# Optimization experiments

Measured on AMD Instinct MI355X. Metric: run time of the kernel, lower is better.

## Reference

```python
import jax, jax.numpy as jnp
import numpy as np

N_HEAD = 16
NEG = -1.0e9


def setup_inputs() -> dict:
    key = jax.random.key(0)
    k1, k2, k3 = jax.random.split(key, 3)
    B, T, C = 4, 2048, 1024
    x = jax.random.normal(k1, (B, T, C), dtype=jnp.float32)
    # torch Linear(C, 3C, bias=False): weight [3C, C], y = x @ W.T
    w_attn = jax.random.normal(k2, (3 * C, C), dtype=jnp.float32) * (1.0 / np.sqrt(C))
    w_proj = jax.random.normal(k3, (C, C), dtype=jnp.float32) * (1.0 / np.sqrt(C))
    return {"x": x, "w_attn": w_attn, "w_proj": w_proj}


def reference(x, w_attn, w_proj):
    B, T, C = x.shape
    hd = C // N_HEAD
    qkv = x @ w_attn.T  # [B,T,3C]
    q, k, v = jnp.split(qkv, 3, axis=2)
    # [B,T,C] -> [B,H,T,hd]
    q = q.reshape(B, T, N_HEAD, hd).transpose(0, 2, 1, 3)
    k = k.reshape(B, T, N_HEAD, hd).transpose(0, 2, 1, 3)
    v = v.reshape(B, T, N_HEAD, hd).transpose(0, 2, 1, 3)
    att = jnp.einsum('bhqd,bhkd->bhqk', q, k) * (1.0 / np.sqrt(hd))
    causal = jnp.tril(jnp.ones((T, T), dtype=bool))
    att = jnp.where(causal[None, None, :, :], att, NEG)
    att = jax.nn.softmax(att, axis=-1)
    y = jnp.einsum('bhqk,bhkd->bhqd', att, v)  # [B,H,T,hd]
    y = y.transpose(0, 2, 1, 3).reshape(B, T, C)
    return y @ w_proj.T
```

## Files before the change

kernel.cpp:

```cpp
#include <hip/hip_runtime.h>
#include <hip/hip_bf16.h>

typedef __bf16 bf16x8_t __attribute__((ext_vector_type(8)));
typedef __bf16 bf16x4_t __attribute__((ext_vector_type(4)));
typedef float f32x4_t __attribute__((ext_vector_type(4)));

__device__ __forceinline__ void gload_lds16(const void* g, void* l) {
    __builtin_amdgcn_global_load_lds((const __attribute__((address_space(1))) void*)g,
                                     (__attribute__((address_space(3))) void*)l, 16, 0, 0);
}

__global__ void f2bf3_kernel(const float* __restrict__ x, const float* __restrict__ wa,
                             const float* __restrict__ wp, __bf16* __restrict__ xb,
                             __bf16* __restrict__ wab, __bf16* __restrict__ wpb) {
    int i = blockIdx.x * blockDim.x + threadIdx.x;
    const float* in; __bf16* out; int off;
    if (i < 2097152)      { in = x;  out = xb;  off = i; }
    else if (i < 2883584) { in = wa; out = wab; off = i - 2097152; }
    else                  { in = wp; out = wpb; off = i - 2883584; }
    float4 v = *(const float4*)(in + off * 4);
    bf16x4_t o;
    o[0] = (__bf16)v.x; o[1] = (__bf16)v.y; o[2] = (__bf16)v.z; o[3] = (__bf16)v.w;
    *(bf16x4_t*)(out + off * 4) = o;
}

__global__ __launch_bounds__(512, 2) void gemm1_m201(const __bf16* __restrict__ A,
                                                     const __bf16* __restrict__ Bt,
                                                     __bf16* __restrict__ Cqk,
                                                     __bf16* __restrict__ Vg,
                                                     int M, int N, int K) {
    __shared__ __bf16 As[2][256 * 64];
    __shared__ __bf16 Bs[2][256 * 64];

    const int tid  = threadIdx.x;
    const int lane = tid & 63;
    const int wid  = tid >> 6;
    const int wm   = wid >> 2;
    const int wn   = wid & 3;

    int fl = blockIdx.x;
    fl = (fl & 7) * (gridDim.x >> 3) + (fl >> 3);
    const int m0 = (fl / 12) * 256;
    const int n0 = (fl % 12) * 256;

    const int lr = lane & 15;
    const int lg = lane >> 4;
    const int cr = lg * 4;
    const int srow = lane >> 3;
    const int gcol = (((lane & 7) ^ srow) << 3);

    f32x4_t acc[8][4];
#pragma unroll
    for (int i = 0; i < 8; ++i)
#pragma unroll
        for (int j = 0; j < 4; ++j)
            acc[i][j] = (f32x4_t){0.f, 0.f, 0.f, 0.f};

    const int NT = K >> 6;
    const int NI = NT >> 1;

    bf16x8_t af[4][2], bf0[2][2], bf1[2][2];

    auto stA = [&](int kt, int buf, int half) {
        const __bf16* Ab = A + (size_t)m0 * K + (size_t)kt * 64;
        const int s0 = half * 16 + wid, s1 = s0 + 8;
        gload_lds16(Ab + (size_t)(s0 * 8 + srow) * K + gcol, &As[buf][s0 * 512]);
        gload_lds16(Ab + (size_t)(s1 * 8 + srow) * K + gcol, &As[buf][s1 * 512]);
    };
    auto stB = [&](int kt, int buf, int half) {
        const __bf16* Bb = Bt + (size_t)n0 * K + (size_t)kt * 64;
        const int s0 = half * 16 + wid, s1 = s0 + 8;
        gload_lds16(Bb + (size_t)(s0 * 8 + srow) * K + gcol, &Bs[buf][s0 * 512]);
        gload_lds16(Bb + (size_t)(s1 * 8 + srow) * K + gcol, &Bs[buf][s1 * 512]);
    };
    auto dsA = [&](const __bf16* Ab, int mfh) {
#pragma unroll
        for (int mf = 0; mf < 4; ++mf)
#pragma unroll
            for (int kk = 0; kk < 2; ++kk) {
                const int row = wm * 128 + (mfh * 4 + mf) * 16 + lr;
                const int g   = kk * 4 + lg;
                af[mf][kk] = *(const bf16x8_t*)&Ab[row * 64 + ((g ^ (row & 7)) << 3)];
            }
    };
    auto dsB = [&](const __bf16* Bb, int nfh, bf16x8_t (&dst)[2][2]) {
#pragma unroll
        for (int nfp = 0; nfp < 2; ++nfp)
#pragma unroll
            for (int kk = 0; kk < 2; ++kk) {
                const int row = wn * 64 + (nfh * 2 + nfp) * 16 + lr;
                const int g   = kk * 4 + lg;
                dst[nfp][kk] = *(const bf16x8_t*)&Bb[row * 64 + ((g ^ (row & 7)) << 3)];
            }
    };
    auto MF = [&](int mfh, bf16x8_t (&bfr)[2][2], int nfh) {
        __builtin_amdgcn_s_setprio(1);
#pragma unroll
        for (int mf = 0; mf < 4; ++mf)
#pragma unroll
            for (int nfp = 0; nfp < 2; ++nfp) {
                const int ai = mfh * 4 + mf, bi = nfh * 2 + nfp;
                acc[ai][bi] = __builtin_amdgcn_mfma_f32_16x16x32_bf16(af[mf][0], bfr[nfp][0], acc[ai][bi], 0, 0, 0);
                acc[ai][bi] = __builtin_amdgcn_mfma_f32_16x16x32_bf16(af[mf][1], bfr[nfp][1], acc[ai][bi], 0, 0, 0);
            }
        __builtin_amdgcn_s_setprio(0);
    };

#define BAR() __builtin_amdgcn_s_barrier()
#define LGK0() asm volatile("s_waitcnt lgkmcnt(0)" ::: "memory")

    stA(0, 0, 0); stA(0, 0, 1); stB(0, 0, 0); stB(0, 0, 1);
    stB(1, 1, 0); stB(1, 1, 1);
    asm volatile("s_waitcnt vmcnt(4)" ::: "memory");
    BAR();

    for (int it = 0; it < NI; ++it) {
        const int t1 = 2 * it + 1, t2 = 2 * it + 2, t3 = 2 * it + 3;
        const bool lastit = (it == NI - 1);

        dsA(As[0], 0); dsB(Bs[0], 0, bf0);
        stA(t1, 1, 0);
        BAR(); LGK0();
        MF(0, bf0, 0);
        BAR();

        dsB(Bs[0], 1, bf1);
        stA(t1, 1, 1);
        BAR(); LGK0();
        MF(0, bf1, 1);
        BAR();

        dsA(As[0], 1);
        if (!lastit) stB(t2, 0, 0);
        BAR(); LGK0();
        MF(1, bf0, 0);
        BAR();

        if (!lastit) stB(t2, 0, 1);
        if (lastit) asm volatile("s_waitcnt vmcnt(0)" ::: "memory");
        else        asm volatile("s_waitcnt vmcnt(4)" ::: "memory");
        BAR();
        MF(1, bf1, 1);
        BAR();

        dsA(As[1], 0); dsB(Bs[1], 0, bf0);
        if (!lastit) stA(t2, 0, 0);
        BAR(); LGK0();
        MF(0, bf0, 0);
        BAR();

        dsB(Bs[1], 1, bf1);
        if (!lastit) stA(t2, 0, 1);
        BAR(); LGK0();
        MF(0, bf1, 1);
        BAR();

        dsA(As[1], 1);
        if (!lastit) stB(t3, 1, 0);
        BAR(); LGK0();
        MF(1, bf0, 0);
        BAR();

        if (!lastit) stB(t3, 1, 1);
        if (lastit) asm volatile("s_waitcnt vmcnt(0)" ::: "memory");
        else        asm volatile("s_waitcnt vmcnt(4)" ::: "memory");
        BAR();
        MF(1, bf1, 1);
        BAR();
    }
#undef BAR
#undef LGK0

    if (n0 < 2048) {
#pragma unroll
        for (int mf = 0; mf < 8; ++mf)
#pragma unroll
            for (int nf = 0; nf < 4; ++nf)
#pragma unroll
                for (int r = 0; r < 4; ++r) {
                    int row = m0 + wm * 128 + mf * 16 + cr + r;
                    int col = n0 + wn * 64 + nf * 16 + lr;
                    Cqk[(size_t)row * 2048 + col] = (__bf16)acc[mf][nf][r];
                }
    } else {
#pragma unroll
        for (int mf = 0; mf < 8; ++mf) {
            const int row0 = m0 + wm * 128 + mf * 16 + cr;
            const int bb   = row0 >> 11;
            const int tt   = row0 & 2047;
#pragma unroll
            for (int nf = 0; nf < 4; ++nf) {
                const int c3 = n0 + wn * 64 + nf * 16 + lr - 2048;
                const int hh = c3 >> 6, dd = c3 & 63;
                bf16x4_t pv;
#pragma unroll
                for (int r = 0; r < 4; ++r) pv[r] = (__bf16)acc[mf][nf][r];
                *(bf16x4_t*)&Vg[((size_t)(bb * 16 + hh) * 64 + dd) * 2048 + tt] = pv;
            }
        }
    }
}

template <typename OutT>
__global__ __launch_bounds__(256) void gemm_bt(const __bf16* __restrict__ A,
                                               const __bf16* __restrict__ Bt,
                                               OutT* __restrict__ C,
                                               int M, int N, int K) {
    __shared__ __bf16 As[128 * 32];
    __shared__ __bf16 Bs[128 * 32];

    const int tid  = threadIdx.x;
    const int lane = tid & 63;
    const int wid  = tid >> 6;
    const int wm   = wid >> 1;
    const int wn   = wid & 1;

    const int nwg = gridDim.x * gridDim.y;
    int fl = blockIdx.y * gridDim.x + blockIdx.x;
    fl = (fl & 7) * (nwg >> 3) + (fl >> 3);
    const int m0 = (fl / gridDim.x) * 128;
    const int n0 = (fl % gridDim.x) * 128;

    const int lr = lane & 15;
    const int lk = (lane >> 4) * 8;
    const int cr = (lane >> 4) * 4;

    f32x4_t acc[4][4];
    for (int i = 0; i < 4; ++i)
        for (int j = 0; j < 4; ++j)
            acc[i][j] = (f32x4_t){0.f, 0.f, 0.f, 0.f};

    for (int k0 = 0; k0 < K; k0 += 32) {
        __syncthreads();
        for (int i = 0; i < 2; ++i) {
            int flat = i * 256 + tid;
            int row  = flat >> 2;
            int col  = (flat & 3) * 8;
            gload_lds16(&A[(size_t)(m0 + row) * K + k0 + col], &As[(size_t)(i * 256 + wid * 64) * 8]);
            gload_lds16(&Bt[(size_t)(n0 + row) * K + k0 + col], &Bs[(size_t)(i * 256 + wid * 64) * 8]);
        }
        __syncthreads();

        bf16x8_t af[4], bfr[4];
        for (int mf = 0; mf < 4; ++mf)
            af[mf] = *(const bf16x8_t*)&As[(wm * 64 + mf * 16 + lr) * 32 + lk];
        for (int nf = 0; nf < 4; ++nf)
            bfr[nf] = *(const bf16x8_t*)&Bs[(wn * 64 + nf * 16 + lr) * 32 + lk];
        for (int mf = 0; mf < 4; ++mf)
            for (int nf = 0; nf < 4; ++nf)
                acc[mf][nf] = __builtin_amdgcn_mfma_f32_16x16x32_bf16(af[mf], bfr[nf], acc[mf][nf], 0, 0, 0);
    }

    for (int mf = 0; mf < 4; ++mf)
        for (int nf = 0; nf < 4; ++nf)
            for (int r = 0; r < 4; ++r) {
                int row = m0 + wm * 64 + mf * 16 + cr + r;
                int col = n0 + wn * 64 + nf * 16 + lr;
                C[(size_t)row * N + col] = (OutT)acc[mf][nf][r];
            }
}

__global__ __launch_bounds__(512, 4) void attn_kernel(const __bf16* __restrict__ qkv,
                                                      const __bf16* __restrict__ Vg,
                                                      __bf16* __restrict__ y) {
    const int T = 2048, LD = 2048;
    const int orig = blockIdx.x;
    const int bidx = ((orig & 7) << 6) + (orig >> 3);
    const int pair = bidx & 7;
    const int h    = (bidx >> 3) & 15;
    const int b    = bidx >> 7;

    __shared__ __bf16 Ks[128 * 64];
    __shared__ __bf16 Vt[64 * 128];
    __shared__ __bf16 Ps[8 * 16 * 136];

    const int tid  = threadIdx.x;
    const int lane = tid & 63;
    const int w    = tid >> 6;
    const int lr   = lane & 15;
    const int lg   = lane >> 4;
    const int lk   = lg * 8;

    const __bf16* qg  = qkv + (size_t)b * T * LD + h * 64;
    const __bf16* kg  = qg + 1024;
    const __bf16* Vgb = Vg + (size_t)(b * 16 + h) * 64 * 2048;

    const float CE    = 0.125f * 1.44269504f;
    const float DEFER = 44.0f;

    const int r0    = tid >> 3;
    const int kcol  = (tid & 7) * 8;
    const int kslot = ((tid & 7) ^ (r0 & 7)) << 3;
    const int vd  = tid >> 3;
    const int vc0 = tid & 7;

    __bf16* Pw = &Ps[w * 16 * 136];

    for (int pass = 0; pass < 2; ++pass) {
        const int qs  = pass ? 15 - pair : pair;
        const int qt0 = qs * 128;
        const int nt  = qs + 1;

        bf16x8_t qf0, qf1;
        {
            const __bf16* qrow = qg + (size_t)(qt0 + w * 16 + lr) * LD;
            qf0 = *(const bf16x8_t*)&qrow[lk];
            qf1 = *(const bf16x8_t*)&qrow[32 + lk];
        }

        bf16x8_t ka = *(const bf16x8_t*)&kg[(size_t)r0 * LD + kcol];
        bf16x8_t kb = *(const bf16x8_t*)&kg[(size_t)(64 + r0) * LD + kcol];
        bf16x8_t va = *(const bf16x8_t*)&Vgb[(size_t)vd * 2048 + vc0 * 8];
        bf16x8_t vb = *(const bf16x8_t*)&Vgb[(size_t)vd * 2048 + (vc0 + 8) * 8];

        f32x4_t o_acc[4];
#pragma unroll
        for (int i = 0; i < 4; ++i) o_acc[i] = (f32x4_t){0.f, 0.f, 0.f, 0.f};
        float m_r = -3.0e38f, l_r = 0.f;

        for (int t = 0; t < nt; ++t) {
            __syncthreads();

            *(bf16x8_t*)&Ks[r0 * 64 + kslot] = ka;
            *(bf16x8_t*)&Ks[(64 + r0) * 64 + kslot] = kb;
            *(bf16x8_t*)&Vt[vd * 128 + ((vc0 ^ (vd & 7)) << 3)] = va;
            *(bf16x8_t*)&Vt[vd * 128 + (((vc0 + 8) ^ (vd & 7)) << 3)] = vb;

            __syncthreads();

            if (t + 1 < nt) {
                const size_t kb0 = (size_t)(t + 1) * 128;
                ka = *(const bf16x8_t*)&kg[(kb0 + r0) * LD + kcol];
                kb = *(const bf16x8_t*)&kg[(kb0 + 64 + r0) * LD + kcol];
                va = *(const bf16x8_t*)&Vgb[(size_t)vd * 2048 + kb0 + vc0 * 8];
                vb = *(const bf16x8_t*)&Vgb[(size_t)vd * 2048 + kb0 + (vc0 + 8) * 8];
            }

            f32x4_t s[8];
            __builtin_amdgcn_s_setprio(1);
#pragma unroll
            for (int c = 0; c < 8; ++c) {
                const int key = c * 16 + lr;
                const int sw  = (key & 7) << 3;
                bf16x8_t kfa = *(const bf16x8_t*)&Ks[key * 64 + (lk ^ sw)];
                bf16x8_t kfb = *(const bf16x8_t*)&Ks[key * 64 + ((32 + lk) ^ sw)];
                s[c] = __builtin_amdgcn_mfma_f32_16x16x32_bf16(kfa, qf0, (f32x4_t){0.f, 0.f, 0.f, 0.f}, 0, 0, 0);
                s[c] = __builtin_amdgcn_mfma_f32_16x16x32_bf16(kfb, qf1, s[c], 0, 0, 0);
            }
            __builtin_amdgcn_s_setprio(0);

            if (t == nt - 1) {
                const int ql = w * 16 + lr;
#pragma unroll
                for (int c = 0; c < 8; ++c)
#pragma unroll
                    for (int r = 0; r < 4; ++r)
                        if (c * 16 + lg * 4 + r > ql) s[c][r] = -1.0e30f;
            }

            float pm = s[0][0];
#pragma unroll
            for (int c = 0; c < 8; ++c)
#pragma unroll
                for (int r = 0; r < 4; ++r) pm = fmaxf(pm, s[c][r]);

            if (!__all(pm <= m_r + DEFER)) {
                pm = fmaxf(pm, __shfl_xor(pm, 16));
                pm = fmaxf(pm, __shfl_xor(pm, 32));
                const float mn    = fmaxf(m_r, pm);
                const float alpha = exp2f((m_r - mn) * CE);
                l_r *= alpha;
#pragma unroll
                for (int dt = 0; dt < 4; ++dt)
#pragma unroll
                    for (int r = 0; r < 4; ++r) o_acc[dt][r] *= alpha;
                m_r = mn;
            }
            const float mce = m_r * CE;

            float rs = 0.f;
#pragma unroll
            for (int c = 0; c < 8; ++c) {
                bf16x4_t pk;
#pragma unroll
                for (int r = 0; r < 4; ++r) {
                    float pv = exp2f(fmaf(s[c][r], CE, -mce));
                    rs += pv;
                    pk[r] = (__bf16)pv;
                }
                *(bf16x4_t*)&Pw[lr * 136 + c * 16 + lg * 4] = pk;
            }
            rs += __shfl_xor(rs, 16);
            rs += __shfl_xor(rs, 32);
            l_r += rs;

            __builtin_amdgcn_s_setprio(1);
#pragma unroll
            for (int hf = 0; hf < 2; ++hf) {
                bf16x8_t pb0 = *(const bf16x8_t*)&Pw[lr * 136 + hf * 64 + lk];
                bf16x8_t pb1 = *(const bf16x8_t*)&Pw[lr * 136 + hf * 64 + 32 + lk];
#pragma unroll
                for (int dt = 0; dt < 4; ++dt) {
                    const int d = dt * 16 + lr;
                    bf16x8_t vb0 = *(const bf16x8_t*)&Vt[d * 128 + (((hf * 8 + lg) ^ (d & 7)) << 3)];
                    bf16x8_t vb1 = *(const bf16x8_t*)&Vt[d * 128 + (((hf * 8 + 4 + lg) ^ (d & 7)) << 3)];
                    o_acc[dt] = __builtin_amdgcn_mfma_f32_16x16x32_bf16(vb0, pb0, o_acc[dt], 0, 0, 0);
                    o_acc[dt] = __builtin_amdgcn_mfma_f32_16x16x32_bf16(vb1, pb1, o_acc[dt], 0, 0, 0);
                }
            }
            __builtin_amdgcn_s_setprio(0);
        }

        const float inv = 1.0f / l_r;
        const int q = qt0 + w * 16 + lr;
#pragma unroll
        for (int dt = 0; dt < 4; ++dt) {
            bf16x4_t ov;
#pragma unroll
            for (int r = 0; r < 4; ++r) ov[r] = (__bf16)(o_acc[dt][r] * inv);
            *(bf16x4_t*)&y[(size_t)(b * T + q) * 1024 + h * 64 + dt * 16 + lg * 4] = ov;
        }
    }
}

extern "C" void kernel_launch(void* const* d_in, const int* in_sizes, int n_in,
                              void* d_out, int out_size, void* d_ws, size_t ws_size,
                              hipStream_t stream) {
    const float* x      = (const float*)d_in[0];
    const float* w_attn = (const float*)d_in[1];
    const float* w_proj = (const float*)d_in[2];
    float* out = (float*)d_out;

    char* ws = (char*)d_ws;
    __bf16* xb   = (__bf16*)(ws);
    __bf16* wab  = (__bf16*)(ws + 16777216);
    __bf16* wpb  = (__bf16*)(ws + 23068672);
    __bf16* qkvb = (__bf16*)(ws + 25165824);
    __bf16* yb   = (__bf16*)(ws + 58720256);
    __bf16* Vg   = (__bf16*)(ws + 75497472);

    f2bf3_kernel<<<12288, 256, 0, stream>>>(x, w_attn, w_proj, xb, wab, wpb);

    gemm1_m201<<<384, 512, 0, stream>>>(xb, wab, qkvb, Vg, 8192, 3072, 1024);

    attn_kernel<<<512, 512, 0, stream>>>(qkvb, Vg, yb);

    gemm_bt<float><<<dim3(8, 64), 256, 0, stream>>>(yb, wpb, out, 8192, 1024, 1024);
}
```

Before: 181.3 us.

## Switch attention to 32x32x16 MFMA with register-resident P via permlane32 swap

Rewrites the attention kernel to use 32x32x16 bf16 MFMAs, with 4 waves of 32 query rows each instead of 8 waves of 16 rows. The probabilities stay in registers: they are packed with v_cvt_pk_bf16_f32 and rearranged with v_permlane32_swap into the B-operand layout, so the LDS P buffer and its write/read round trip are gone. The aim is fewer LDS operations and syncs per tile and denser matrix-core use. In exchange each wave holds more registers (16-wide accumulators), the block has fewer threads, and each thread issues more global loads.

```diff
diff --git a/kernel.cpp b/kernel.cpp
--- a/kernel.cpp
+++ b/kernel.cpp
@@ -4,10 +4,17 @@
 typedef __bf16 bf16x8_t __attribute__((ext_vector_type(8)));
 typedef __bf16 bf16x4_t __attribute__((ext_vector_type(4)));
 typedef float f32x4_t __attribute__((ext_vector_type(4)));
+typedef float f32x16_t __attribute__((ext_vector_type(16)));
 
 __device__ __forceinline__ void gload_lds16(const void* g, void* l) {
     __builtin_amdgcn_global_load_lds((const __attribute__((address_space(1))) void*)g,
                                      (__attribute__((address_space(3))) void*)l, 16, 0, 0);
+}
+
+__device__ __forceinline__ unsigned pk_bf16(float a, float b) {
+    unsigned r;
+    asm("v_cvt_pk_bf16_f32 %0, %1, %2" : "=v"(r) : "v"(a), "v"(b));
+    return r;
 }
 
 __global__ void f2bf3_kernel(const float* __restrict__ x, const float* __restrict__ wa,
@@ -260,7 +267,7 @@
             }
 }
 
-__global__ __launch_bounds__(512, 4) void attn_kernel(const __bf16* __restrict__ qkv,
+__global__ __launch_bounds__(256, 2) void attn_kernel(const __bf16* __restrict__ qkv,
                                                       const __bf16* __restrict__ Vg,
                                                       __bf16* __restrict__ y) {
     const int T = 2048, LD = 2048;
@@ -272,14 +279,12 @@
 
     __shared__ __bf16 Ks[128 * 64];
     __shared__ __bf16 Vt[64 * 128];
-    __shared__ __bf16 Ps[8 * 16 * 136];
 
     const int tid  = threadIdx.x;
     const int lane = tid & 63;
     const int w    = tid >> 6;
-    const int lr   = lane & 15;
-    const int lg   = lane >> 4;
-    const int lk   = lg * 8;
+    const int l31  = lane & 31;
+    const int hi   = lane >> 5;
 
     const __bf16* qg  = qkv + (size_t)b * T * LD + h * 64;
     const __bf16* kg  = qg + 1024;
@@ -288,137 +293,153 @@
     const float CE    = 0.125f * 1.44269504f;
     const float DEFER = 44.0f;
 
-    const int r0    = tid >> 3;
-    const int kcol  = (tid & 7) * 8;
-    const int kslot = ((tid & 7) ^ (r0 & 7)) << 3;
-    const int vd  = tid >> 3;
-    const int vc0 = tid & 7;
-
-    __bf16* Pw = &Ps[w * 16 * 136];
+    const int kc = tid & 7;
+    const int kr8 = tid >> 3;
+    const int kslot = (kc ^ (kr8 & 7)) << 3;
+    const int vc = tid & 15;
+    const int vd8 = tid >> 4;
+    const int vslot = (vc ^ (vd8 & 7)) << 3;
 
     for (int pass = 0; pass < 2; ++pass) {
         const int qs  = pass ? 15 - pair : pair;
         const int qt0 = qs * 128;
         const int nt  = qs + 1;
-
-        bf16x8_t qf0, qf1;
-        {
-            const __bf16* qrow = qg + (size_t)(qt0 + w * 16 + lr) * LD;
-            qf0 = *(const bf16x8_t*)&qrow[lk];
-            qf1 = *(const bf16x8_t*)&qrow[32 + lk];
-        }
-
-        bf16x8_t ka = *(const bf16x8_t*)&kg[(size_t)r0 * LD + kcol];
-        bf16x8_t kb = *(const bf16x8_t*)&kg[(size_t)(64 + r0) * LD + kcol];
-        bf16x8_t va = *(const bf16x8_t*)&Vgb[(size_t)vd * 2048 + vc0 * 8];
-        bf16x8_t vb = *(const bf16x8_t*)&Vgb[(size_t)vd * 2048 + (vc0 + 8) * 8];
-
-        f32x4_t o_acc[4];
-#pragma unroll
-        for (int i = 0; i < 4; ++i) o_acc[i] = (f32x4_t){0.f, 0.f, 0.f, 0.f};
+        const int qgl = qt0 + w * 32 + l31;
+
+        bf16x8_t qreg[4];
+#pragma unroll
+        for (int ks = 0; ks < 4; ++ks)
+            qreg[ks] = *(const bf16x8_t*)&qg[(size_t)qgl * LD + ks * 16 + 8 * hi];
+
+        bf16x8_t kreg[4], vreg[4];
+#pragma unroll
+        for (int jj = 0; jj < 4; ++jj)
+            kreg[jj] = *(const bf16x8_t*)&kg[(size_t)(kr8 + 32 * jj) * LD + kc * 8];
+#pragma unroll
+        for (int jj = 0; jj < 4; ++jj)
+            vreg[jj] = *(const bf16x8_t*)&Vgb[(size_t)(vd8 + 16 * jj) * 2048 + vc * 8];
+
+        f32x16_t o0 = (f32x16_t)(0.f), o1 = (f32x16_t)(0.f);
         float m_r = -3.0e38f, l_r = 0.f;
 
         for (int t = 0; t < nt; ++t) {
             __syncthreads();
 
-            *(bf16x8_t*)&Ks[r0 * 64 + kslot] = ka;
-            *(bf16x8_t*)&Ks[(64 + r0) * 64 + kslot] = kb;
-            *(bf16x8_t*)&Vt[vd * 128 + ((vc0 ^ (vd & 7)) << 3)] = va;
-            *(bf16x8_t*)&Vt[vd * 128 + (((vc0 + 8) ^ (vd & 7)) << 3)] = vb;
+#pragma unroll
+            for (int jj = 0; jj < 4; ++jj)
+                *(bf16x8_t*)&Ks[(kr8 + 32 * jj) * 64 + kslot] = kreg[jj];
+#pragma unroll
+            for (int jj = 0; jj < 4; ++jj)
+                *(bf16x8_t*)&Vt[(vd8 + 16 * jj) * 128 + vslot] = vreg[jj];
 
             __syncthreads();
 
             if (t + 1 < nt) {
                 const size_t kb0 = (size_t)(t + 1) * 128;
-                ka = *(const bf16x8_t*)&kg[(kb0 + r0) * LD + kcol];
-                kb = *(const bf16x8_t*)&kg[(kb0 + 64 + r0) * LD + kcol];
-                va = *(const bf16x8_t*)&Vgb[(size_t)vd * 2048 + kb0 + vc0 * 8];
-                vb = *(const bf16x8_t*)&Vgb[(size_t)vd * 2048 + kb0 + (vc0 + 8) * 8];
-            }
-
-            f32x4_t s[8];
+#pragma unroll
+                for (int jj = 0; jj < 4; ++jj)
+                    kreg[jj] = *(const bf16x8_t*)&kg[(kb0 + kr8 + 32 * jj) * LD + kc * 8];
+#pragma unroll
+                for (int jj = 0; jj < 4; ++jj)
+                    vreg[jj] = *(const bf16x8_t*)&Vgb[(size_t)(vd8 + 16 * jj) * 2048 + kb0 + vc * 8];
+            }
+
+            f32x16_t s[4];
             __builtin_amdgcn_s_setprio(1);
 #pragma unroll
-            for (int c = 0; c < 8; ++c) {
-                const int key = c * 16 + lr;
-                const int sw  = (key & 7) << 3;
-                bf16x8_t kfa = *(const bf16x8_t*)&Ks[key * 64 + (lk ^ sw)];
-                bf16x8_t kfb = *(const bf16x8_t*)&Ks[key * 64 + ((32 + lk) ^ sw)];
-                s[c] = __builtin_amdgcn_mfma_f32_16x16x32_bf16(kfa, qf0, (f32x4_t){0.f, 0.f, 0.f, 0.f}, 0, 0, 0);
-                s[c] = __builtin_amdgcn_mfma_f32_16x16x32_bf16(kfb, qf1, s[c], 0, 0, 0);
+            for (int kb = 0; kb < 4; ++kb) {
+                const int key = kb * 32 + l31;
+                const int sw7 = key & 7;
+                s[kb] = (f32x16_t)(0.f);
+#pragma unroll
+                for (int ks = 0; ks < 4; ++ks) {
+                    bf16x8_t kf = *(const bf16x8_t*)&Ks[key * 64 + (((2 * ks + hi) ^ sw7) << 3)];
+                    s[kb] = __builtin_amdgcn_mfma_f32_32x32x16_bf16(kf, qreg[ks], s[kb], 0, 0, 0);
+                }
             }
             __builtin_amdgcn_s_setprio(0);
 
             if (t == nt - 1) {
-                const int ql = w * 16 + lr;
-#pragma unroll
-                for (int c = 0; c < 8; ++c)
-#pragma unroll
-                    for (int r = 0; r < 4; ++r)
-                        if (c * 16 + lg * 4 + r > ql) s[c][r] = -1.0e30f;
+                const int ql = w * 32 + l31;
+#pragma unroll
+                for (int kb = 0; kb < 4; ++kb)
+#pragma unroll
+                    for (int r = 0; r < 16; ++r) {
+                        const int key = kb * 32 + (r & 3) + 8 * (r >> 2) + 4 * hi;
+                        if (key > ql) s[kb][r] = -1.0e30f;
+                    }
             }
 
             float pm = s[0][0];
 #pragma unroll
-            for (int c = 0; c < 8; ++c)
-#pragma unroll
-                for (int r = 0; r < 4; ++r) pm = fmaxf(pm, s[c][r]);
+            for (int kb = 0; kb < 4; ++kb)
+#pragma unroll
+                for (int r = 0; r < 16; ++r) pm = fmaxf(pm, s[kb][r]);
 
             if (!__all(pm <= m_r + DEFER)) {
-                pm = fmaxf(pm, __shfl_xor(pm, 16));
                 pm = fmaxf(pm, __shfl_xor(pm, 32));
                 const float mn    = fmaxf(m_r, pm);
                 const float alpha = exp2f((m_r - mn) * CE);
                 l_r *= alpha;
 #pragma unroll
-                for (int dt = 0; dt < 4; ++dt)
-#pragma unroll
-                    for (int r = 0; r < 4; ++r) o_acc[dt][r] *= alpha;
+                for (int r = 0; r < 16; ++r) { o0[r] *= alpha; o1[r] *= alpha; }
                 m_r = mn;
             }
             const float mce = m_r * CE;
 
             float rs = 0.f;
 #pragma unroll
-            for (int c = 0; c < 8; ++c) {
-                bf16x4_t pk;
-#pragma unroll
-                for (int r = 0; r < 4; ++r) {
-                    float pv = exp2f(fmaf(s[c][r], CE, -mce));
+            for (int kb = 0; kb < 4; ++kb)
+#pragma unroll
+                for (int r = 0; r < 16; ++r) {
+                    float pv = exp2f(fmaf(s[kb][r], CE, -mce));
+                    s[kb][r] = pv;
                     rs += pv;
-                    pk[r] = (__bf16)pv;
                 }
-                *(bf16x4_t*)&Pw[lr * 136 + c * 16 + lg * 4] = pk;
-            }
-            rs += __shfl_xor(rs, 16);
             rs += __shfl_xor(rs, 32);
             l_r += rs;
 
             __builtin_amdgcn_s_setprio(1);
 #pragma unroll
-            for (int hf = 0; hf < 2; ++hf) {
-                bf16x8_t pb0 = *(const bf16x8_t*)&Pw[lr * 136 + hf * 64 + lk];
-                bf16x8_t pb1 = *(const bf16x8_t*)&Pw[lr * 136 + hf * 64 + 32 + lk];
-#pragma unroll
-                for (int dt = 0; dt < 4; ++dt) {
-                    const int d = dt * 16 + lr;
-                    bf16x8_t vb0 = *(const bf16x8_t*)&Vt[d * 128 + (((hf * 8 + lg) ^ (d & 7)) << 3)];
-                    bf16x8_t vb1 = *(const bf16x8_t*)&Vt[d * 128 + (((hf * 8 + 4 + lg) ^ (d & 7)) << 3)];
-                    o_acc[dt] = __builtin_amdgcn_mfma_f32_16x16x32_bf16(vb0, pb0, o_acc[dt], 0, 0, 0);
-                    o_acc[dt] = __builtin_amdgcn_mfma_f32_16x16x32_bf16(vb1, pb1, o_acc[dt], 0, 0, 0);
+            for (int ks = 0; ks < 8; ++ks) {
+                const int kb = ks >> 1;
+                const int rb = 8 * (ks & 1);
+                unsigned L0 = pk_bf16(s[kb][rb + 0], s[kb][rb + 1]);
+                unsigned L1 = pk_bf16(s[kb][rb + 2], s[kb][rb + 3]);
+                unsigned H0 = pk_bf16(s[kb][rb + 4], s[kb][rb + 5]);
+                unsigned H1 = pk_bf16(s[kb][rb + 6], s[kb][rb + 7]);
+                asm("v_permlane32_swap_b32 %0, %1" : "+v"(L0), "+v"(H0));
+                asm("v_permlane32_swap_b32 %0, %1" : "+v"(L1), "+v"(H1));
+                union { unsigned u[4]; bf16x8_t v; } uf;
+                uf.u[0] = L0; uf.u[1] = L1; uf.u[2] = H0; uf.u[3] = H1;
+                const int gv = 2 * ks + hi;
+                {
+                    const int d = l31;
+                    bf16x8_t vf = *(const bf16x8_t*)&Vt[d * 128 + ((gv ^ (d & 7)) << 3)];
+                    o0 = __builtin_amdgcn_mfma_f32_32x32x16_bf16(vf, uf.v, o0, 0, 0, 0);
+                }
+                {
+                    const int d = 32 + l31;
+                    bf16x8_t vf = *(const bf16x8_t*)&Vt[d * 128 + ((gv ^ (d & 7)) << 3)];
+                    o1 = __builtin_amdgcn_mfma_f32_32x32x16_bf16(vf, uf.v, o1, 0, 0, 0);
                 }
             }
             __builtin_amdgcn_s_setprio(0);
         }
 
         const float inv = 1.0f / l_r;
-        const int q = qt0 + w * 16 + lr;
-#pragma unroll
-        for (int dt = 0; dt < 4; ++dt) {
-            bf16x4_t ov;
-#pragma unroll
-            for (int r = 0; r < 4; ++r) ov[r] = (__bf16)(o_acc[dt][r] * inv);
-            *(bf16x4_t*)&y[(size_t)(b * T + q) * 1024 + h * 64 + dt * 16 + lg * 4] = ov;
+        __bf16* yrow = y + (size_t)(b * T + qgl) * 1024 + h * 64;
+#pragma unroll
+        for (int tq = 0; tq < 4; ++tq) {
+            bf16x4_t ov0, ov1;
+#pragma unroll
+            for (int u = 0; u < 4; ++u) {
+                ov0[u] = (__bf16)(o0[tq * 4 + u] * inv);
+                ov1[u] = (__bf16)(o1[tq * 4 + u] * inv);
+            }
+            const int dl = 8 * tq + 4 * hi;
+            *(bf16x4_t*)&yrow[dl]      = ov0;
+            *(bf16x4_t*)&yrow[32 + dl] = ov1;
         }
     }
 }
@@ -443,7 +464,7 @@
 
     gemm1_m201<<<384, 512, 0, stream>>>(xb, wab, qkvb, Vg, 8192, 3072, 1024);
 
-    attn_kernel<<<512, 512, 0, stream>>>(qkvb, Vg, yb);
+    attn_kernel<<<512, 256, 0, stream>>>(qkvb, Vg, yb);
 
     gemm_bt<float><<<dim3(8, 64), 256, 0, stream>>>(yb, wpb, out, 8192, 1024, 1024);
 }
```

Result: no change. 177.8 us (-1.9%).
